# Kernel tuning notes

Hardware: AMD Instinct MI355X
Metric: run time of the kernel (lower is better)

The kernel has to match this reference:

```python
import jax, jax.numpy as jnp
import numpy as np

L = 2          # n_blocks
E = 512        # emb
H = 8          # heads
D = E // H     # head dim
T = 4096       # context_len
V = 32000      # vocab_size
WIN = 16       # one-sided window (k)
FF = 4 * E     # ff_hidden_mult * emb
EPS = 1e-5


def setup_inputs() -> dict:
    key = jax.random.key(0)
    ks = jax.random.split(key, 12)
    s = 0.02
    return {
        'tokens': jax.random.randint(ks[0], (2, T), 0, V, dtype=jnp.int32),
        'attention_mask': jnp.ones((2, T), dtype=jnp.int32),
        'tok_emb': jax.random.normal(ks[1], (V, E), jnp.float32) * s,
        'pos_emb': jax.random.normal(ks[2], (T, E), jnp.float32) * s,
        'Wq': jax.random.normal(ks[3], (L, E, E), jnp.float32) * s,
        'Wk': jax.random.normal(ks[4], (L, E, E), jnp.float32) * s,
        'Wv': jax.random.normal(ks[5], (L, E, E), jnp.float32) * s,
        'Wo': jax.random.normal(ks[6], (L, E, E), jnp.float32) * s,
        'bo': jnp.zeros((L, E), jnp.float32),
        'ln1_g': jnp.ones((L, E), jnp.float32),
        'ln1_b': jnp.zeros((L, E), jnp.float32),
        'ln2_g': jnp.ones((L, E), jnp.float32),
        'ln2_b': jnp.zeros((L, E), jnp.float32),
        'W1': jax.random.normal(ks[7], (L, E, FF), jnp.float32) * s,
        'b1': jnp.zeros((L, FF), jnp.float32),
        'W2': jax.random.normal(ks[8], (L, FF, E), jnp.float32) * s,
        'b2': jnp.zeros((L, E), jnp.float32),
    }


def layer_norm(x, g, b):
    m = jnp.mean(x, axis=-1, keepdims=True)
    v = jnp.mean(jnp.square(x - m), axis=-1, keepdims=True)
    return (x - m) * jax.lax.rsqrt(v + EPS) * g + b


def sliding_window_attn(x, mask, Wq, Wk, Wv, Wo, bo):
    # x: [B,T,E], mask: [B,T] int
    B, Tt, _ = x.shape
    q = (x @ Wq).reshape(B, Tt, H, D)
    k = (x @ Wk).reshape(B, Tt, H, D)
    v = (x @ Wv).reshape(B, Tt, H, D)
    idx = jnp.arange(Tt)[:, None] + jnp.arange(-WIN, WIN + 1)[None, :]
    valid = (idx >= 0) & (idx < Tt)
    idxc = jnp.clip(idx, 0, Tt - 1)
    kg = k[:, idxc]
    vg = v[:, idxc]
    scores = jnp.einsum('bthd,btwhd->bhtw', q, kg) / jnp.sqrt(jnp.asarray(D, x.dtype))
    mvalid = valid[None, :, :] & (mask[:, idxc] > 0)
    scores = jnp.where(mvalid[:, None, :, :], scores, jnp.asarray(-1e9, x.dtype))
    a = jax.nn.softmax(scores, axis=-1)
    out = jnp.einsum('bhtw,btwhd->bthd', a, vg).reshape(B, Tt, E)
    return out @ Wo + bo


def reference(tokens, attention_mask, tok_emb, pos_emb, Wq, Wk, Wv, Wo, bo,
              ln1_g, ln1_b, ln2_g, ln2_b, W1, b1, W2, b2):
    x = tok_emb[tokens] + pos_emb[None, :, :]             # embed + learned pos
    for l in range(L):
        h = layer_norm(x, ln1_g[l], ln1_b[l])
        x = x + sliding_window_attn(h, attention_mask, Wq[l], Wk[l], Wv[l], Wo[l], bo[l])
        h = layer_norm(x, ln2_g[l], ln2_b[l])
        x = x + (jax.nn.relu(h @ W1[l] + b1[l]) @ W2[l] + b2[l])
    return x
```

## Files before the change

### kernel.cpp

```cpp
#include <hip/hip_runtime.h>

typedef unsigned short u16;
typedef unsigned int u32;
typedef __bf16 bf16x8 __attribute__((ext_vector_type(8)));
typedef float f32x4 __attribute__((ext_vector_type(4)));
typedef u16 u16x8 __attribute__((ext_vector_type(8)));

#define T_SEQ 4096
#define E_DIM 512
#define H_HEADS 8
#define FF_DIM 2048
#define BATCH 2
#define MROWS (BATCH * T_SEQ)

__device__ __forceinline__ float bf2f(u16 u) {
  union { u32 i; float f; } w; w.i = ((u32)u) << 16; return w.f;
}
__device__ __forceinline__ u16 f2bf(float f) {
  union { float f; u32 i; } w; w.f = f;
  u32 r = w.i + 0x7FFFu + ((w.i >> 16) & 1u);
  return (u16)(r >> 16);
}
__device__ __forceinline__ void gload_lds16(const void* g, void* l) {
  __builtin_amdgcn_global_load_lds(
      (const __attribute__((address_space(1))) void*)g,
      (__attribute__((address_space(3))) void*)l, 16, 0, 0);
}

__global__ __launch_bounds__(256) void wconv_kernel(
    const float* __restrict__ Wq, const float* __restrict__ Wk,
    const float* __restrict__ Wv, const float* __restrict__ Wo,
    const float* __restrict__ W1, const float* __restrict__ W2,
    u16* __restrict__ wqkv_t, u16* __restrict__ wo_t,
    u16* __restrict__ w1_t, u16* __restrict__ w2_t) {
  const int z = blockIdx.y;
  const int l = z / 6, ty = z % 6;
  const float* in; u16* op; int K, N;
  const size_t EE = (size_t)E_DIM * E_DIM;
  const size_t EF = (size_t)E_DIM * FF_DIM;
  switch (ty) {
    case 0: in = Wq + l * EE; op = wqkv_t + l * 3 * EE;          K = E_DIM;  N = E_DIM;  break;
    case 1: in = Wk + l * EE; op = wqkv_t + l * 3 * EE + EE;     K = E_DIM;  N = E_DIM;  break;
    case 2: in = Wv + l * EE; op = wqkv_t + l * 3 * EE + 2 * EE; K = E_DIM;  N = E_DIM;  break;
    case 3: in = Wo + l * EE; op = wo_t + l * EE;                K = E_DIM;  N = E_DIM;  break;
    case 4: in = W1 + l * EF; op = w1_t + l * EF;                K = E_DIM;  N = FF_DIM; break;
    default:in = W2 + l * EF; op = w2_t + l * EF;                K = FF_DIM; N = E_DIM;  break;
  }
  const int nn = N >> 5;
  const int ntile = (K >> 5) * nn;
  const int tile = blockIdx.x;
  if (tile >= ntile) return;
  const int tk = tile / nn, tn = tile % nn;
  __shared__ float tl[32][33];
  const int tx = threadIdx.x & 31, tr = threadIdx.x >> 5;
#pragma unroll
  for (int i = 0; i < 4; i++)
    tl[tr + i * 8][tx] = in[(size_t)(tk * 32 + tr + i * 8) * N + tn * 32 + tx];
  __syncthreads();
#pragma unroll
  for (int i = 0; i < 4; i++)
    op[(size_t)(tn * 32 + tr + i * 8) * K + tk * 32 + tx] = f2bf(tl[tx][tr + i * 8]);
}

__global__ __launch_bounds__(256) void embed_kernel(
    const int* __restrict__ tokens, const float* __restrict__ tok_emb,
    const float* __restrict__ pos_emb, float* __restrict__ x) {
  const int idx = blockIdx.x * 256 + threadIdx.x;
  const int rowi = idx >> 7, c4 = (idx & 127) * 4;
  const int t = rowi & (T_SEQ - 1);
  const int tok = tokens[rowi];
  float4 e = *(const float4*)(tok_emb + (size_t)tok * E_DIM + c4);
  float4 p = *(const float4*)(pos_emb + (size_t)t * E_DIM + c4);
  e.x += p.x; e.y += p.y; e.z += p.z; e.w += p.w;
  *(float4*)(x + (size_t)rowi * E_DIM + c4) = e;
}

__global__ __launch_bounds__(256) void ln_kernel(
    const float* __restrict__ x, const float* __restrict__ gam,
    const float* __restrict__ bet, u16* __restrict__ out) {
  const int row = blockIdx.x * 4 + (threadIdx.x >> 6);
  const int lane = threadIdx.x & 63;
  const float* xr = x + (size_t)row * E_DIM + lane * 8;
  float4 v0 = *(const float4*)xr;
  float4 v1 = *(const float4*)(xr + 4);
  float s  = v0.x + v0.y + v0.z + v0.w + v1.x + v1.y + v1.z + v1.w;
  float s2 = v0.x * v0.x + v0.y * v0.y + v0.z * v0.z + v0.w * v0.w +
             v1.x * v1.x + v1.y * v1.y + v1.z * v1.z + v1.w * v1.w;
#pragma unroll
  for (int o = 32; o; o >>= 1) { s += __shfl_xor(s, o); s2 += __shfl_xor(s2, o); }
  const float mean = s * (1.f / E_DIM);
  const float var = s2 * (1.f / E_DIM) - mean * mean;
  const float inv = rsqrtf(var + 1e-5f);
  float4 g0 = *(const float4*)(gam + lane * 8);
  float4 g1 = *(const float4*)(gam + lane * 8 + 4);
  float4 b0 = *(const float4*)(bet + lane * 8);
  float4 b1 = *(const float4*)(bet + lane * 8 + 4);
  u16x8 o8;
  o8[0] = f2bf((v0.x - mean) * inv * g0.x + b0.x);
  o8[1] = f2bf((v0.y - mean) * inv * g0.y + b0.y);
  o8[2] = f2bf((v0.z - mean) * inv * g0.z + b0.z);
  o8[3] = f2bf((v0.w - mean) * inv * g0.w + b0.w);
  o8[4] = f2bf((v1.x - mean) * inv * g1.x + b1.x);
  o8[5] = f2bf((v1.y - mean) * inv * g1.y + b1.y);
  o8[6] = f2bf((v1.z - mean) * inv * g1.z + b1.z);
  o8[7] = f2bf((v1.w - mean) * inv * g1.w + b1.w);
  *(u16x8*)(out + (size_t)row * E_DIM + lane * 8) = o8;
}

template <int BM, int BN, bool BIAS, bool RELU, bool RESID, bool OUTBF>
__global__ __launch_bounds__(256) void gemm_nt(
    const u16* __restrict__ A, const u16* __restrict__ Bt,
    const float* __restrict__ bias, const float* __restrict__ resid,
    void* __restrict__ outp, int K, int N, int gx) {
  constexpr int BK = 64;
  constexpr int FM = BM / 32, FN = BN / 32;
  __shared__ __align__(16) u16 As[2][BM * BK];
  __shared__ __align__(16) u16 Bs[2][BN * BK];
  const int tid = threadIdx.x;
  const int wave = tid >> 6, lane = tid & 63;

  const int cpx = gridDim.x >> 3;
  const int bid = blockIdx.x;
  const int sw = (bid & 7) * cpx + (bid >> 3);
  const int bx = sw % gx, by = sw / gx;

  const int m0 = by * BM, n0 = bx * BN;
  const int wr = wave >> 1, wc = wave & 1;
  const int r = lane & 15, g = lane >> 4;

  const int srow = lane >> 3;
  const int scol = (lane & 7) ^ srow;

  f32x4 acc[FM][FN];
#pragma unroll
  for (int i = 0; i < FM; i++)
#pragma unroll
    for (int j = 0; j < FN; j++) acc[i][j] = (f32x4){0.f, 0.f, 0.f, 0.f};

  constexpr int ASEG = BM / 8, BSEG = BN / 8;

  auto stage = [&](int buf, int k0) {
#pragma unroll
    for (int s = wave; s < ASEG; s += 4) {
      const u16* gp = A + (size_t)(m0 + s * 8 + srow) * K + k0 + scol * 8;
      gload_lds16(gp, (char*)As[buf] + s * 1024 + lane * 16);
    }
#pragma unroll
    for (int s = wave; s < BSEG; s += 4) {
      const u16* gp = Bt + (size_t)(n0 + s * 8 + srow) * K + k0 + scol * 8;
      gload_lds16(gp, (char*)Bs[buf] + s * 1024 + lane * 16);
    }
  };

  auto compute = [&](int buf) {
#pragma unroll
    for (int kk = 0; kk < BK; kk += 32) {
      bf16x8 av[FM], bv[FN];
      const int cg = (kk >> 3) + g;
#pragma unroll
      for (int i = 0; i < FM; i++) {
        const int row = wr * (BM / 2) + i * 16 + r;
        av[i] = *reinterpret_cast<const bf16x8*>(
            &As[buf][row * 64 + ((cg ^ (row & 7)) << 3)]);
      }
#pragma unroll
      for (int j = 0; j < FN; j++) {
        const int row = wc * (BN / 2) + j * 16 + r;
        bv[j] = *reinterpret_cast<const bf16x8*>(
            &Bs[buf][row * 64 + ((cg ^ (row & 7)) << 3)]);
      }
      __builtin_amdgcn_s_setprio(1);
#pragma unroll
      for (int i = 0; i < FM; i++)
#pragma unroll
        for (int j = 0; j < FN; j++)
          acc[i][j] = __builtin_amdgcn_mfma_f32_16x16x32_bf16(av[i], bv[j], acc[i][j], 0, 0, 0);
      __builtin_amdgcn_s_setprio(0);
    }
  };

  const int NT = K >> 6;
  int cur = 0;
  stage(0, 0);
  __syncthreads();
  for (int t = 0; t < NT - 1; ++t) {
    stage(cur ^ 1, (t + 1) << 6);
    compute(cur);
    __syncthreads();
    cur ^= 1;
  }
  compute(cur);

#pragma unroll
  for (int i = 0; i < FM; i++) {
#pragma unroll
    for (int j = 0; j < FN; j++) {
      const int col = n0 + wc * (BN / 2) + j * 16 + r;
      const float bc = BIAS ? bias[col] : 0.f;
#pragma unroll
      for (int rr = 0; rr < 4; rr++) {
        const int row = m0 + wr * (BM / 2) + i * 16 + g * 4 + rr;
        float v = acc[i][j][rr] + bc;
        if (RELU) v = fmaxf(v, 0.f);
        if (RESID) v += resid[(size_t)row * N + col];
        if (OUTBF) ((u16*)outp)[(size_t)row * N + col] = f2bf(v);
        else       ((float*)outp)[(size_t)row * N + col] = v;
      }
    }
  }
}

__global__ __launch_bounds__(256) void attn_kernel(
    const u16* __restrict__ qkv, const int* __restrict__ mask,
    u16* __restrict__ out) {
  __shared__ __align__(16) u16 Vt[64][128];
  __shared__ __align__(16) u16 Pl[4][16][72];
  __shared__ int ml[96];
  const int b = blockIdx.y >> 3, h = blockIdx.y & 7;
  const int t0 = blockIdx.x * 64;
  const int tid = threadIdx.x;
  const int wave = tid >> 6, lane = tid & 63;
  const int q15 = lane & 15, g = lane >> 4;

  for (int s = tid; s < 112 * 8; s += 256) {
    const int c = s >> 3, seg = s & 7;
    u16x8 v8 = {0, 0, 0, 0, 0, 0, 0, 0};
    const int kt = t0 - 16 + c;
    if (c < 96 && kt >= 0 && kt < T_SEQ)
      v8 = *(const u16x8*)(qkv + (size_t)(b * T_SEQ + kt) * 1536 + 1024 + h * 64 + seg * 8);
#pragma unroll
    for (int j = 0; j < 8; j++) {
      const int d = seg * 8 + j;
      const int cp = (c & 7) | ((((c >> 3) ^ seg) & 15) << 3);
      Vt[d][cp] = v8[j];
    }
  }
  for (int i = tid; i < 96; i += 256) {
    const int kt = t0 - 16 + i;
    ml[i] = (kt >= 0 && kt < T_SEQ) ? mask[b * T_SEQ + kt] : 0;
  }

  const size_t qrow = (size_t)(b * T_SEQ + t0 + wave * 16 + q15) * 1536 + h * 64;
  bf16x8 qf[2];
  qf[0] = *(const bf16x8*)(qkv + qrow + g * 8);
  qf[1] = *(const bf16x8*)(qkv + qrow + 32 + g * 8);
  bf16x8 kf[3][2];
#pragma unroll
  for (int mt = 0; mt < 3; mt++) {
    int kt = t0 - 16 + wave * 16 + mt * 16 + q15;
    kt = kt < 0 ? 0 : (kt >= T_SEQ ? T_SEQ - 1 : kt);
    const size_t kr = (size_t)(b * T_SEQ + kt) * 1536 + 512 + h * 64;
    kf[mt][0] = *(const bf16x8*)(qkv + kr + g * 8);
    kf[mt][1] = *(const bf16x8*)(qkv + kr + 32 + g * 8);
  }

  f32x4 sa[3];
#pragma unroll
  for (int mt = 0; mt < 3; mt++) sa[mt] = (f32x4){0.f, 0.f, 0.f, 0.f};
#pragma unroll
  for (int ks = 0; ks < 2; ks++)
#pragma unroll
    for (int mt = 0; mt < 3; mt++)
      sa[mt] = __builtin_amdgcn_mfma_f32_16x16x32_bf16(kf[mt][ks], qf[ks], sa[mt], 0, 0, 0);

  __syncthreads();

  float p[12];
  float mx = -1e30f;
#pragma unroll
  for (int mt = 0; mt < 3; mt++)
#pragma unroll
    for (int rr = 0; rr < 4; rr++) {
      const int cl = mt * 16 + g * 4 + rr;
      const bool ok = (cl >= q15) && (cl <= q15 + 32) && (ml[wave * 16 + cl] != 0);
      const float s = ok ? sa[mt][rr] * 0.125f : -1e9f;
      p[mt * 4 + rr] = s;
      mx = fmaxf(mx, s);
    }
  mx = fmaxf(mx, __shfl_xor(mx, 16));
  mx = fmaxf(mx, __shfl_xor(mx, 32));
  float sum = 0.f;
#pragma unroll
  for (int i = 0; i < 12; i++) { p[i] = __expf(p[i] - mx); sum += p[i]; }
  sum += __shfl_xor(sum, 16);
  sum += __shfl_xor(sum, 32);
  const float inv = 1.f / sum;

  u16* prow = &Pl[wave][q15][0];
#pragma unroll
  for (int mt = 0; mt < 3; mt++) {
    const u32 w0 = (u32)f2bf(p[mt * 4 + 0] * inv) | ((u32)f2bf(p[mt * 4 + 1] * inv) << 16);
    const u32 w1 = (u32)f2bf(p[mt * 4 + 2] * inv) | ((u32)f2bf(p[mt * 4 + 3] * inv) << 16);
    *(u32*)(prow + mt * 16 + g * 4) = w0;
    *(u32*)(prow + mt * 16 + g * 4 + 2) = w1;
  }
  *(u32*)(prow + 48 + g * 4) = 0;
  *(u32*)(prow + 48 + g * 4 + 2) = 0;

  f32x4 oa[4];
#pragma unroll
  for (int nt = 0; nt < 4; nt++) oa[nt] = (f32x4){0.f, 0.f, 0.f, 0.f};
#pragma unroll
  for (int ks = 0; ks < 2; ks++) {
    const bf16x8 pa = *(const bf16x8*)(&Pl[wave][q15][ks * 32 + g * 8]);
#pragma unroll
    for (int nt = 0; nt < 4; nt++) {
      const int d = nt * 16 + q15;
      const int chunk = 2 * wave + 4 * ks + g;
      const int cp = ((chunk ^ ((d >> 3) & 7)) & 15) << 3;
      const bf16x8 vb = *(const bf16x8*)(&Vt[d][cp]);
      oa[nt] = __builtin_amdgcn_mfma_f32_16x16x32_bf16(pa, vb, oa[nt], 0, 0, 0);
    }
  }

  u16* orow = out + (size_t)(b * T_SEQ + t0 + wave * 16) * E_DIM + h * 64;
#pragma unroll
  for (int nt = 0; nt < 4; nt++)
#pragma unroll
    for (int rr = 0; rr < 4; rr++)
      orow[(size_t)(g * 4 + rr) * E_DIM + nt * 16 + q15] = f2bf(oa[nt][rr]);
}

extern "C" void kernel_launch(void* const* d_in, const int* in_sizes, int n_in,
                              void* d_out, int out_size, void* d_ws, size_t ws_size,
                              hipStream_t stream) {
  const int*   tokens   = (const int*)d_in[0];
  const int*   attnmask = (const int*)d_in[1];
  const float* tok_emb  = (const float*)d_in[2];
  const float* pos_emb  = (const float*)d_in[3];
  const float* Wq       = (const float*)d_in[4];
  const float* Wk       = (const float*)d_in[5];
  const float* Wv       = (const float*)d_in[6];
  const float* Wo       = (const float*)d_in[7];
  const float* bo       = (const float*)d_in[8];
  const float* ln1_g    = (const float*)d_in[9];
  const float* ln1_b    = (const float*)d_in[10];
  const float* ln2_g    = (const float*)d_in[11];
  const float* ln2_b    = (const float*)d_in[12];
  const float* W1       = (const float*)d_in[13];
  const float* b1       = (const float*)d_in[14];
  const float* W2       = (const float*)d_in[15];
  const float* b2       = (const float*)d_in[16];
  float* x = (float*)d_out;

  u16* wqkv_t  = (u16*)d_ws;
  u16* wo_t    = wqkv_t + 2 * 1536 * 512;
  u16* w1_t    = wo_t + 2 * 512 * 512;
  u16* w2_t    = w1_t + 2 * 2048 * 512;
  u16* h_bf    = w2_t + 2 * 512 * 2048;
  u16* qkv_bf  = h_bf + (size_t)MROWS * 512;
  u16* attn_bf = qkv_bf + (size_t)MROWS * 1536;
  u16* mid_bf  = attn_bf + (size_t)MROWS * 512;

  wconv_kernel<<<dim3(1024, 12), 256, 0, stream>>>(Wq, Wk, Wv, Wo, W1, W2,
                                                   wqkv_t, wo_t, w1_t, w2_t);
  embed_kernel<<<dim3(4096), 256, 0, stream>>>(tokens, tok_emb, pos_emb, x);

  for (int l = 0; l < 2; l++) {
    const size_t EE = (size_t)512 * 512;
    const size_t EF = (size_t)512 * 2048;
    ln_kernel<<<dim3(2048), 256, 0, stream>>>(x, ln1_g + l * 512, ln1_b + l * 512, h_bf);
    gemm_nt<128, 128, false, false, false, true>
        <<<dim3(768), 256, 0, stream>>>(h_bf, wqkv_t + l * 3 * EE,
                                        nullptr, nullptr, qkv_bf, 512, 1536, 12);
    attn_kernel<<<dim3(64, 16), 256, 0, stream>>>(qkv_bf, attnmask, attn_bf);
    gemm_nt<64, 128, true, false, true, false>
        <<<dim3(512), 256, 0, stream>>>(attn_bf, wo_t + l * EE,
                                        bo + l * 512, x, x, 512, 512, 4);
    ln_kernel<<<dim3(2048), 256, 0, stream>>>(x, ln2_g + l * 512, ln2_b + l * 512, h_bf);
    gemm_nt<128, 128, true, true, false, true>
        <<<dim3(1024), 256, 0, stream>>>(h_bf, w1_t + l * EF,
                                         b1 + l * 2048, nullptr, mid_bf, 512, 2048, 16);
    gemm_nt<64, 128, true, false, true, false>
        <<<dim3(512), 256, 0, stream>>>(mid_bf, w2_t + l * EF,
                                        b2 + l * 512, x, x, 2048, 512, 4);
  }
}
```

Measured before the change: 377.5 us.

## Replace double-buffered GEMM staging with single-buffer load-sync-compute loop

Removes the double-buffered LDS prefetch in the GEMM kernel and replaces it with a single buffer that is loaded, synchronized, then computed on each K step. This halves shared memory per block, which may allow more resident blocks per CU, and simplifies the loop. In exchange, global-to-LDS loads no longer overlap with MFMA compute within a block and a second barrier is added per iteration.

```diff
diff --git a/kernel.cpp b/kernel.cpp
--- a/kernel.cpp
+++ b/kernel.cpp
@@ -114,8 +114,8 @@
     void* __restrict__ outp, int K, int N, int gx) {
   constexpr int BK = 64;
   constexpr int FM = BM / 32, FN = BN / 32;
-  __shared__ __align__(16) u16 As[2][BM * BK];
-  __shared__ __align__(16) u16 Bs[2][BN * BK];
+  __shared__ __align__(16) u16 As[BM * BK];
+  __shared__ __align__(16) u16 Bs[BN * BK];
   const int tid = threadIdx.x;
   const int wave = tid >> 6, lane = tid & 63;
 
@@ -139,20 +139,21 @@
 
   constexpr int ASEG = BM / 8, BSEG = BN / 8;
 
-  auto stage = [&](int buf, int k0) {
-#pragma unroll
-    for (int s = wave; s < ASEG; s += 4) {
+  for (int k0 = 0; k0 < K; k0 += BK) {
+    __syncthreads();
+#pragma unroll
+    for (int i = 0; i < ASEG / 4; i++) {
+      const int s = i * 4 + wave;
       const u16* gp = A + (size_t)(m0 + s * 8 + srow) * K + k0 + scol * 8;
-      gload_lds16(gp, (char*)As[buf] + s * 1024 + lane * 16);
-    }
-#pragma unroll
-    for (int s = wave; s < BSEG; s += 4) {
+      gload_lds16(gp, (char*)As + s * 1024 + lane * 16);
+    }
+#pragma unroll
+    for (int i = 0; i < BSEG / 4; i++) {
+      const int s = i * 4 + wave;
       const u16* gp = Bt + (size_t)(n0 + s * 8 + srow) * K + k0 + scol * 8;
-      gload_lds16(gp, (char*)Bs[buf] + s * 1024 + lane * 16);
-    }
-  };
-
-  auto compute = [&](int buf) {
+      gload_lds16(gp, (char*)Bs + s * 1024 + lane * 16);
+    }
+    __syncthreads();
 #pragma unroll
     for (int kk = 0; kk < BK; kk += 32) {
       bf16x8 av[FM], bv[FN];
@@ -161,13 +162,13 @@
       for (int i = 0; i < FM; i++) {
         const int row = wr * (BM / 2) + i * 16 + r;
         av[i] = *reinterpret_cast<const bf16x8*>(
-            &As[buf][row * 64 + ((cg ^ (row & 7)) << 3)]);
+            &As[row * 64 + ((cg ^ (row & 7)) << 3)]);
       }
 #pragma unroll
       for (int j = 0; j < FN; j++) {
         const int row = wc * (BN / 2) + j * 16 + r;
         bv[j] = *reinterpret_cast<const bf16x8*>(
-            &Bs[buf][row * 64 + ((cg ^ (row & 7)) << 3)]);
+            &Bs[row * 64 + ((cg ^ (row & 7)) << 3)]);
       }
       __builtin_amdgcn_s_setprio(1);
 #pragma unroll
@@ -177,19 +178,7 @@
           acc[i][j] = __builtin_amdgcn_mfma_f32_16x16x32_bf16(av[i], bv[j], acc[i][j], 0, 0, 0);
       __builtin_amdgcn_s_setprio(0);
     }
-  };
-
-  const int NT = K >> 6;
-  int cur = 0;
-  stage(0, 0);
-  __syncthreads();
-  for (int t = 0; t < NT - 1; ++t) {
-    stage(cur ^ 1, (t + 1) << 6);
-    compute(cur);
-    __syncthreads();
-    cur ^= 1;
-  }
-  compute(cur);
+  }
 
 #pragma unroll
   for (int i = 0; i < FM; i++) {
```

Result: no change. 373.7 us (-1.0%).
